# Performance work log

Hardware: AMD Instinct MI355X
Metric: run time of the kernel (lower is better)

Reference implementation:

```python
import jax, jax.numpy as jnp
import numpy as np

N_NODES = 50000
N_EDGES = 800000
N_GRAPHS = 512
IN_DIM = 50
H = 128  # hidden_channels


def _init_linear(key, out_dim, in_dim, bias=True):
    k1, k2 = jax.random.split(key)
    bound = 1.0 / np.sqrt(in_dim)
    W = jax.random.uniform(k1, (out_dim, in_dim), jnp.float32, -bound, bound)
    if bias:
        b = jax.random.uniform(k2, (out_dim,), jnp.float32, -bound, bound)
        return W, b
    return W


def setup_inputs() -> dict:
    key = jax.random.key(0)
    ks = jax.random.split(key, 16)
    x = jax.random.normal(ks[0], (N_NODES, IN_DIM), jnp.float32)
    edge_index = jax.random.randint(ks[1], (2, N_EDGES), 0, N_NODES, jnp.int64)
    batch = jnp.sort(jax.random.randint(ks[2], (N_NODES,), 0, N_GRAPHS, jnp.int64))
    Wl1, bl1 = _init_linear(ks[3], H, IN_DIM)
    Wr1 = _init_linear(ks[4], H, IN_DIM, bias=False)
    Wl2, bl2 = _init_linear(ks[5], 2 * H, H)
    Wr2 = _init_linear(ks[6], 2 * H, H, bias=False)
    Wl3, bl3 = _init_linear(ks[7], 4 * H, 2 * H)
    Wr3 = _init_linear(ks[8], 4 * H, 2 * H, bias=False)
    Wf1, bf1 = _init_linear(ks[9], 2 * H, 4 * H)
    Wf2, bf2 = _init_linear(ks[10], H, 2 * H)
    Wo, bo = _init_linear(ks[11], 1, H)
    return dict(x=x, edge_index=edge_index, batch=batch,
                Wl1=Wl1, bl1=bl1, Wr1=Wr1,
                Wl2=Wl2, bl2=bl2, Wr2=Wr2,
                Wl3=Wl3, bl3=bl3, Wr3=Wr3,
                Wf1=Wf1, bf1=bf1, Wf2=Wf2, bf2=bf2, Wo=Wo, bo=bo)


def sage_conv(x, src, dst, deg_inv, Wl, bl, Wr):
    # mean-aggregate neighbor features at destination nodes, then linear
    agg = jax.ops.segment_sum(x[src], dst, num_segments=N_NODES) * deg_inv
    return agg @ Wl.T + bl + x @ Wr.T


def reference(x, edge_index, batch, Wl1, bl1, Wr1, Wl2, bl2, Wr2,
              Wl3, bl3, Wr3, Wf1, bf1, Wf2, bf2, Wo, bo):
    src, dst = edge_index[0], edge_index[1]
    deg = jax.ops.segment_sum(jnp.ones((N_EDGES,), x.dtype), dst, num_segments=N_NODES)
    deg_inv = (1.0 / jnp.maximum(deg, 1.0))[:, None]

    x1 = jax.nn.leaky_relu(sage_conv(x, src, dst, deg_inv, Wl1, bl1, Wr1))
    x2 = jax.nn.relu(sage_conv(x1, src, dst, deg_inv, Wl2, bl2, Wr2))
    x3 = jax.nn.relu(sage_conv(x2, src, dst, deg_inv, Wl3, bl3, Wr3))

    # global mean pool per graph
    pool_sum = jax.ops.segment_sum(x3, batch, num_segments=N_GRAPHS)
    cnt = jax.ops.segment_sum(jnp.ones((N_NODES,), x.dtype), batch, num_segments=N_GRAPHS)
    x_pool = pool_sum / jnp.maximum(cnt, 1.0)[:, None]

    x4 = jax.nn.relu(x_pool @ Wf1.T + bf1)
    x5 = jax.nn.relu(x4 @ Wf2.T + bf2)
    return jax.nn.sigmoid(x5 @ Wo.T + bo)
```

## Files before the change

### kernel.cpp

```cpp
#include <hip/hip_runtime.h>
#include <math.h>

#define N_NODES 50000
#define N_EDGES 800000
#define N_GRAPHS 512
#define M_PAD 50176
#define SEG_SZ 6250
#define EPT 8
#define SEG_BLOCKS 391
#define FILL_BLOCKS (SEG_BLOCKS * 8)
#define CAP 64

typedef unsigned char u8;
typedef unsigned short u16;
typedef unsigned int u32;
typedef long i64;
using floatx4 = __attribute__((ext_vector_type(4))) float;
using floatx2 = __attribute__((ext_vector_type(2))) float;

__device__ __forceinline__ u8 f2fp8(float v) {
    return (u8)(__builtin_amdgcn_cvt_pk_fp8_f32(v, v, 0, false) & 0xFF);
}
__device__ __forceinline__ u32 pack4fp8(float a, float b, float c, float d) {
    u32 p = __builtin_amdgcn_cvt_pk_fp8_f32(a, b, 0, false);
    return __builtin_amdgcn_cvt_pk_fp8_f32(c, d, p, true);
}
__device__ __forceinline__ void acc16fp8p(floatx2* acc2, uint4 u) {
    const u32 w[4] = {u.x, u.y, u.z, u.w};
    #pragma unroll
    for (int j = 0; j < 4; ++j) {
        acc2[j * 2 + 0] += __builtin_amdgcn_cvt_pk_f32_fp8((int)w[j], false);
        acc2[j * 2 + 1] += __builtin_amdgcn_cvt_pk_f32_fp8((int)w[j], true);
    }
}

__device__ __forceinline__ void load_lds16(const u8* g, u8* l) {
    __builtin_amdgcn_global_load_lds(
        (const __attribute__((address_space(1))) u32*)g,
        (__attribute__((address_space(3))) u32*)l, 16, 0, 0);
}
template<int N> __device__ __forceinline__ void waitcnt_vm() {
    __builtin_amdgcn_s_waitcnt(0x0F70 | N);
}
__device__ __forceinline__ void raw_barrier() {
    asm volatile("s_barrier" ::: "memory");
}

__global__ __launch_bounds__(256) void prep_kernel(
    const int* __restrict__ src, const int* __restrict__ dst,
    int* __restrict__ cursor, u16* __restrict__ csr,
    const int* __restrict__ batch, int* __restrict__ gstart,
    const float* __restrict__ x,
    const float* __restrict__ Wl1, const float* __restrict__ Wr1,
    const float* __restrict__ Wl2, const float* __restrict__ Wr2,
    const float* __restrict__ Wl3, const float* __restrict__ Wr3,
    const float* __restrict__ Wf1, const float* __restrict__ Wf2,
    u8* __restrict__ abuf1,
    u8* __restrict__ wb1, u8* __restrict__ wb2, u8* __restrict__ wb3,
    float* __restrict__ Wf1T, float* __restrict__ Wf2T)
{
    if (blockIdx.x < FILL_BLOCKS) {
        const int seg = blockIdx.x & 7;
        const int lo = seg * SEG_SZ, hi = lo + SEG_SZ;
        int e = (blockIdx.x >> 3) * (256 * EPT) + threadIdx.x;
        #pragma unroll
        for (int j = 0; j < EPT; ++j, e += 256) {
            if (e < N_EDGES) {
                int d = dst[e];
                if (d >= lo && d < hi) {
                    int p = atomicAdd(&cursor[d], 1);
                    csr[d * CAP + p] = (u16)src[e];
                }
            }
        }
        return;
    }
    const int bx = blockIdx.x - FILL_BLOCKS;
    if (bx < 196) {
        int i = bx * 256 + threadIdx.x;
        if (i >= N_NODES) return;
        int b = batch[i];
        int bp = (i == 0) ? -1 : batch[i - 1];
        for (int g = bp + 1; g <= b; ++g) gstart[g] = i;
        if (i == N_NODES - 1)
            for (int g = b + 1; g <= N_GRAPHS; ++g) gstart[g] = N_NODES;
        return;
    }
    int i = (bx - 196) * 256 + threadIdx.x;
    if (i < N_NODES * 16) {
        int n = i >> 4, c = (i & 15) * 4;
        float v[4];
        #pragma unroll
        for (int j = 0; j < 4; ++j) {
            int cc = c + j;
            v[j] = (cc < 50) ? x[n * 50 + cc] : 0.0f;
        }
        *(u32*)(abuf1 + (size_t)n * 128 + 64 + c) = pack4fp8(v[0], v[1], v[2], v[3]);
        return;
    }
    i -= N_NODES * 16;
    if (i < 128 * 64) {
        int o = i / 64, c = i % 64;
        float vl = (c < 50) ? Wl1[o * 50 + c] : 0.0f;
        float vr = (c < 50) ? Wr1[o * 50 + c] : 0.0f;
        wb1[(size_t)o * 128 + c] = f2fp8(vl);
        wb1[(size_t)o * 128 + 64 + c] = f2fp8(vr);
        return;
    }
    i -= 128 * 64;
    if (i < 256 * 128) {
        int o = i / 128, c = i % 128;
        wb2[(size_t)o * 256 + c] = f2fp8(Wl2[o * 128 + c]);
        wb2[(size_t)o * 256 + 128 + c] = f2fp8(Wr2[o * 128 + c]);
        return;
    }
    i -= 256 * 128;
    if (i < 512 * 256) {
        int o = i / 256, c = i % 256;
        wb3[(size_t)o * 512 + c] = f2fp8(Wl3[o * 256 + c]);
        wb3[(size_t)o * 512 + 256 + c] = f2fp8(Wr3[o * 256 + c]);
        return;
    }
    i -= 512 * 256;
    if (i < 256 * 512) {
        int o = i >> 9, k = i & 511;
        Wf1T[(size_t)k * 256 + o] = Wf1[(size_t)o * 512 + k];
        return;
    }
    i -= 256 * 512;
    if (i < 128 * 256) {
        int o = i >> 8, k = i & 255;
        Wf2T[(size_t)k * 128 + o] = Wf2[(size_t)o * 256 + k];
    }
}

template<int DINP>
__global__ __launch_bounds__(256) void csr_agg_kernel(const int* __restrict__ cnt,
                                                      const u16* __restrict__ csr,
                                                      u8* __restrict__ abuf) {
    constexpr int STRIDE = 2 * DINP;
    constexpr int LPR = DINP / 16;
    constexpr int EPW = 64 / LPR;
    const int wave = threadIdx.x >> 6, lane = threadIdx.x & 63;
    const int n = blockIdx.x * 4 + wave;
    if (n >= N_NODES) return;
    const int sub = lane / LPR;
    const int li = lane % LPR;
    const int deg = cnt[n];
    const int s0 = n * CAP, s1 = s0 + deg;

    floatx2 acc2[8] = {};
    const u8* xin = abuf + DINP;

    int e = s0 + sub;
    for (; e + EPW < s1; e += 2 * EPW) {
        int i0 = csr[e], i1 = csr[e + EPW];
        uint4 u0 = *(const uint4*)(xin + (size_t)i0 * STRIDE + li * 16);
        uint4 u1 = *(const uint4*)(xin + (size_t)i1 * STRIDE + li * 16);
        acc16fp8p(acc2, u0);
        acc16fp8p(acc2, u1);
    }
    for (; e < s1; e += EPW) {
        int i0 = csr[e];
        uint4 u0 = *(const uint4*)(xin + (size_t)i0 * STRIDE + li * 16);
        acc16fp8p(acc2, u0);
    }

    #pragma unroll
    for (int off = 32; off >= LPR; off >>= 1) {
        #pragma unroll
        for (int c = 0; c < 8; ++c) {
            floatx2 o;
            o[0] = __shfl_down(acc2[c][0], off);
            o[1] = __shfl_down(acc2[c][1], off);
            acc2[c] += o;
        }
    }

    if (lane < LPR) {
        float sc = 1.0f / fmaxf((float)deg, 1.0f);
        uint4 o;
        o.x = pack4fp8(acc2[0][0] * sc, acc2[0][1] * sc, acc2[1][0] * sc, acc2[1][1] * sc);
        o.y = pack4fp8(acc2[2][0] * sc, acc2[2][1] * sc, acc2[3][0] * sc, acc2[3][1] * sc);
        o.z = pack4fp8(acc2[4][0] * sc, acc2[4][1] * sc, acc2[5][0] * sc, acc2[5][1] * sc);
        o.w = pack4fp8(acc2[6][0] * sc, acc2[6][1] * sc, acc2[7][0] * sc, acc2[7][1] * sc);
        *(uint4*)(abuf + (size_t)n * STRIDE + li * 16) = o;
    }
}

template<int K, int NB, int ACT>
__global__ __launch_bounds__(256) void gemm_fp8_kernel(
    const u8* __restrict__ A, const u8* __restrict__ W,
    const float* __restrict__ bias,
    u8* __restrict__ out8, int gstride, int goff, int N)
{
    constexpr int NKB = K / 32;
    constexpr int MT = M_PAD / 128;
    constexpr int MCHUNK = MT / 8;
    __shared__ __align__(16) u8 As[3][128 * 32];
    __shared__ __align__(16) u8 Bs[3][128 * 32];

    const int bx = blockIdx.x;
    const int xcd = bx & 7;
    const int seq = bx >> 3;
    const int n = seq % NB;
    const int m = xcd * MCHUNK + seq / NB;
    if (m >= MT) return;
    const int bm = m * 128;
    const int bn = n * 128;

    const int tid = threadIdx.x;
    const int wave = tid >> 6, lane = tid & 63;
    const int wm = (wave & 1) * 64, wn = (wave >> 1) * 64;
    const int lm = lane & 15, lq = lane >> 4;

    const int srow = wave * 32 + (lane >> 1);
    const int scol = ((lane & 1) ^ ((lane >> 3) & 1)) * 16;
    const u8* gA = A + (size_t)(bm + srow) * K + scol;
    const u8* gB = W + (size_t)(bn + srow) * K + scol;
    const int lbase = wave * 32 * 32;

    auto stage = [&](int s, int r) {
        const int ko = s * 32;
        load_lds16(gA + ko, &As[r][lbase]);
        load_lds16(gB + ko, &Bs[r][lbase]);
    };

    floatx4 acc[4][4] = {};

    stage(0, 0);
    stage(1, 1);

    const int csw = (((lq >> 1) ^ ((lm >> 2) & 1)) << 4) + (lq & 1) * 8;

    #pragma unroll
    for (int kb = 0; kb < NKB; ++kb) {
        if (kb + 2 < NKB) stage(kb + 2, (kb + 2) % 3);
        const int rem = NKB - 1 - kb;
        if (rem >= 2)      waitcnt_vm<4>();
        else if (rem == 1) waitcnt_vm<2>();
        else               waitcnt_vm<0>();
        raw_barrier();

        const int r = kb % 3;
        i64 af[4], bfr[4];
        #pragma unroll
        for (int mi = 0; mi < 4; ++mi)
            af[mi] = *(const i64*)&As[r][(wm + mi * 16 + lm) * 32 + csw];
        #pragma unroll
        for (int ni = 0; ni < 4; ++ni)
            bfr[ni] = *(const i64*)&Bs[r][(wn + ni * 16 + lm) * 32 + csw];
        #pragma unroll
        for (int mi = 0; mi < 4; ++mi)
            #pragma unroll
            for (int ni = 0; ni < 4; ++ni)
                acc[mi][ni] = __builtin_amdgcn_mfma_f32_16x16x32_fp8_fp8(
                    af[mi], bfr[ni], acc[mi][ni], 0, 0, 0);
        raw_barrier();
    }

    #pragma unroll
    for (int mi = 0; mi < 4; ++mi) {
        int node0 = bm + wm + mi * 16 + lq * 4;
        #pragma unroll
        for (int ni = 0; ni < 4; ++ni) {
            int o = bn + wn + ni * 16 + lm;
            float bi = bias[o];
            #pragma unroll
            for (int r = 0; r < 4; ++r) {
                int node = node0 + r;
                if (node >= N) continue;
                float v = acc[mi][ni][r] + bi;
                if (ACT == 0) v = (v > 0.0f) ? v : 0.01f * v;
                else          v = fmaxf(v, 0.0f);
                out8[(size_t)node * gstride + goff + o] = f2fp8(v);
            }
        }
    }
}

template<int K, int NB, int ACT>
__global__ __launch_bounds__(256) void gemm64_fp8_kernel(
    const u8* __restrict__ A, const u8* __restrict__ W,
    const float* __restrict__ bias,
    u8* __restrict__ out8, int gstride, int goff, int N)
{
    constexpr int NKB = K / 64;
    constexpr int MT = M_PAD / 128;
    constexpr int MCHUNK = MT / 8;
    __shared__ __align__(16) u8 As[3][128 * 64];
    __shared__ __align__(16) u8 Bs[3][128 * 64];

    const int bx = blockIdx.x;
    const int xcd = bx & 7;
    const int seq = bx >> 3;
    const int n = seq % NB;
    const int m = xcd * MCHUNK + seq / NB;
    if (m >= MT) return;
    const int bm = m * 128;
    const int bn = n * 128;

    const int tid = threadIdx.x;
    const int wave = tid >> 6, lane = tid & 63;
    const int wm = (wave & 1) * 64, wn = (wave >> 1) * 64;
    const int lm = lane & 15, lq = lane >> 4;

    const int srow = wave * 16 + (lane >> 2);
    const int scd  = ((lane & 3) ^ ((srow >> 1) & 3)) << 4;
    const u8* gA = A + (size_t)(bm + srow) * K + scd;
    const u8* gB = W + (size_t)(bn + srow) * K + scd;
    const int lbase = wave * 1024;

    auto stage = [&](int s, int r) {
        const int ko = s * 64;
        load_lds16(gA + ko,                    &As[r][lbase]);
        load_lds16(gA + (size_t)64 * K + ko,   &As[r][lbase + 4096]);
        load_lds16(gB + ko,                    &Bs[r][lbase]);
        load_lds16(gB + (size_t)64 * K + ko,   &Bs[r][lbase + 4096]);
    };

    floatx4 acc[4][4] = {};

    stage(0, 0);
    stage(1, 1);

    const int pr = (lm >> 1) & 3;
    const int c0 = (((lq >> 1) ^ pr) << 4)       + ((lq & 1) << 3);
    const int c1 = (((2 + (lq >> 1)) ^ pr) << 4) + ((lq & 1) << 3);

    #pragma unroll
    for (int kb = 0; kb < NKB; ++kb) {
        if (kb + 2 < NKB) stage(kb + 2, (kb + 2) % 3);
        const int rem = NKB - 1 - kb;
        if (rem >= 2)      waitcnt_vm<8>();
        else if (rem == 1) waitcnt_vm<4>();
        else               waitcnt_vm<0>();
        raw_barrier();

        const int r = kb % 3;
        i64 af[4][2], bfr[4][2];
        #pragma unroll
        for (int mi = 0; mi < 4; ++mi) {
            const int base = (wm + mi * 16 + lm) * 64;
            af[mi][0] = *(const i64*)&As[r][base + c0];
            af[mi][1] = *(const i64*)&As[r][base + c1];
        }
        #pragma unroll
        for (int ni = 0; ni < 4; ++ni) {
            const int base = (wn + ni * 16 + lm) * 64;
            bfr[ni][0] = *(const i64*)&Bs[r][base + c0];
            bfr[ni][1] = *(const i64*)&Bs[r][base + c1];
        }
        #pragma unroll
        for (int mi = 0; mi < 4; ++mi)
            #pragma unroll
            for (int ni = 0; ni < 4; ++ni) {
                acc[mi][ni] = __builtin_amdgcn_mfma_f32_16x16x32_fp8_fp8(
                    af[mi][0], bfr[ni][0], acc[mi][ni], 0, 0, 0);
                acc[mi][ni] = __builtin_amdgcn_mfma_f32_16x16x32_fp8_fp8(
                    af[mi][1], bfr[ni][1], acc[mi][ni], 0, 0, 0);
            }
        raw_barrier();
    }

    #pragma unroll
    for (int mi = 0; mi < 4; ++mi) {
        int node0 = bm + wm + mi * 16 + lq * 4;
        #pragma unroll
        for (int ni = 0; ni < 4; ++ni) {
            int o = bn + wn + ni * 16 + lm;
            float bi = bias[o];
            #pragma unroll
            for (int r = 0; r < 4; ++r) {
                int node = node0 + r;
                if (node >= N) continue;
                float v = acc[mi][ni][r] + bi;
                if (ACT == 0) v = (v > 0.0f) ? v : 0.01f * v;
                else          v = fmaxf(v, 0.0f);
                out8[(size_t)node * gstride + goff + o] = f2fp8(v);
            }
        }
    }
}

__global__ __launch_bounds__(256) void pool_kernel(
    const u8* __restrict__ x3, const int* __restrict__ gstart,
    float* __restrict__ pool)
{
    __shared__ float sacc[32][128];
    const int g = blockIdx.x >> 2;
    const int slab = blockIdx.x & 3;
    const int t = threadIdx.x;
    const int chain = t >> 3;
    const int li = t & 7;
    const int c0 = slab * 128 + li * 16;
    const int n0 = gstart[g], n1 = gstart[g + 1];

    floatx2 acc2[8] = {};
    for (int n = n0 + chain; n < n1; n += 32) {
        uint4 u = *(const uint4*)(x3 + (size_t)n * 512 + c0);
        acc16fp8p(acc2, u);
    }
    #pragma unroll
    for (int c = 0; c < 8; ++c) {
        sacc[chain][li * 16 + c * 2 + 0] = acc2[c][0];
        sacc[chain][li * 16 + c * 2 + 1] = acc2[c][1];
    }
    __syncthreads();
    if (t < 128) {
        float s = 0.0f;
        #pragma unroll
        for (int r = 0; r < 32; ++r) s += sacc[r][t];
        pool[(size_t)g * 512 + slab * 128 + t] = s;
    }
}

__global__ __launch_bounds__(256) void dense_head_kernel(
    const float* __restrict__ pool, const int* __restrict__ gstart,
    const float* __restrict__ Wf1T, const float* __restrict__ bf1,
    const float* __restrict__ Wf2T, const float* __restrict__ bf2,
    const float* __restrict__ Wo,  const float* __restrict__ bo,
    float* __restrict__ out)
{
    __shared__ float sp[4][512];
    __shared__ float s4[4][256];
    __shared__ float red[128][4];
    const int g0 = blockIdx.x * 4;
    const int t = threadIdx.x;

    #pragma unroll
    for (int g = 0; g < 4; ++g) {
        float sc = 1.0f / fmaxf((float)(gstart[g0 + g + 1] - gstart[g0 + g]), 1.0f);
        sp[g][t]       = pool[(size_t)(g0 + g) * 512 + t] * sc;
        sp[g][t + 256] = pool[(size_t)(g0 + g) * 512 + 256 + t] * sc;
    }
    __syncthreads();

    {
        float s[4];
        #pragma unroll
        for (int g = 0; g < 4; ++g) s[g] = bf1[t];
        #pragma unroll 8
        for (int k = 0; k < 512; ++k) {
            float w = Wf1T[(size_t)k * 256 + t];
            #pragma unroll
            for (int g = 0; g < 4; ++g) s[g] += sp[g][k] * w;
        }
        #pragma unroll
        for (int g = 0; g < 4; ++g) s4[g][t] = fmaxf(s[g], 0.0f);
    }
    __syncthreads();
    if (t < 128) {
        float s[4];
        #pragma unroll
        for (int g = 0; g < 4; ++g) s[g] = bf2[t];
        #pragma unroll 8
        for (int k = 0; k < 256; ++k) {
            float w = Wf2T[(size_t)k * 128 + t];
            #pragma unroll
            for (int g = 0; g < 4; ++g) s[g] += s4[g][k] * w;
        }
        float wo = Wo[t];
        #pragma unroll
        for (int g = 0; g < 4; ++g) red[t][g] = fmaxf(s[g], 0.0f) * wo;
    }
    __syncthreads();
    for (int off = 64; off >= 1; off >>= 1) {
        if (t < off) {
            #pragma unroll
            for (int g = 0; g < 4; ++g) red[t][g] += red[t + off][g];
        }
        __syncthreads();
    }
    if (t < 4) out[g0 + t] = 1.0f / (1.0f + expf(-(red[0][t] + bo[0])));
}

extern "C" void kernel_launch(void* const* d_in, const int* in_sizes, int n_in,
                              void* d_out, int out_size, void* d_ws, size_t ws_size,
                              hipStream_t stream)
{
    const float* x     = (const float*)d_in[0];
    const int*   ei    = (const int*)  d_in[1];
    const int*   batch = (const int*)  d_in[2];
    const float* Wl1   = (const float*)d_in[3];
    const float* bl1   = (const float*)d_in[4];
    const float* Wr1   = (const float*)d_in[5];
    const float* Wl2   = (const float*)d_in[6];
    const float* bl2   = (const float*)d_in[7];
    const float* Wr2   = (const float*)d_in[8];
    const float* Wl3   = (const float*)d_in[9];
    const float* bl3   = (const float*)d_in[10];
    const float* Wr3   = (const float*)d_in[11];
    const float* Wf1   = (const float*)d_in[12];
    const float* bf1   = (const float*)d_in[13];
    const float* Wf2   = (const float*)d_in[14];
    const float* bf2   = (const float*)d_in[15];
    const float* Wo    = (const float*)d_in[16];
    const float* bo    = (const float*)d_in[17];

    const int* src = ei;
    const int* dst = ei + N_EDGES;

    char* p = (char*)d_ws;
    auto alloc = [&](size_t bytes) { char* r = p; p += (bytes + 255) & ~(size_t)255; return r; };
    int*   gstart = (int*)  alloc(513 * 4);
    float* pool   = (float*)alloc((size_t)512 * 512 * 4);
    float* Wf1T   = (float*)alloc((size_t)512 * 256 * 4);
    float* Wf2T   = (float*)alloc((size_t)256 * 128 * 4);
    u8*    abuf1  = (u8*)   alloc((size_t)M_PAD * 128);
    u8*    abuf2  = (u8*)   alloc((size_t)M_PAD * 256);
    u8*    abuf3  = (u8*)   alloc((size_t)M_PAD * 512);
    u8*    x3buf8 = (u8*)   alloc((size_t)M_PAD * 512);
    u8*    wb1    = (u8*)   alloc((size_t)128 * 128);
    u8*    wb2    = (u8*)   alloc((size_t)256 * 256);
    u8*    wb3    = (u8*)   alloc((size_t)512 * 512);
    int*   cursor = (int*)  alloc(50176 * 4);
    u16*   csr    = (u16*)  alloc((size_t)50176 * CAP * 2);

    hipMemsetAsync(cursor, 0, 50176 * 4, stream);
    const int CONV_N = N_NODES * 16 + 128 * 64 + 256 * 128 + 512 * 256
                     + 256 * 512 + 128 * 256;
    const int CONV_BLOCKS = (CONV_N + 255) / 256;
    prep_kernel<<<FILL_BLOCKS + 196 + CONV_BLOCKS, 256, 0, stream>>>(
        src, dst, cursor, csr,
        batch, gstart, x, Wl1, Wr1, Wl2, Wr2, Wl3, Wr3, Wf1, Wf2,
        abuf1, wb1, wb2, wb3, Wf1T, Wf2T);

    const int GB = 12500;
    const int GEMM_GRID = 49 * 8;

    csr_agg_kernel<64><<<GB, 256, 0, stream>>>(cursor, csr, abuf1);
    gemm_fp8_kernel<128, 1, 0><<<GEMM_GRID * 1, 256, 0, stream>>>(
        abuf1, wb1, bl1, abuf2, 256, 128, N_NODES);

    csr_agg_kernel<128><<<GB, 256, 0, stream>>>(cursor, csr, abuf2);
    gemm64_fp8_kernel<256, 2, 1><<<GEMM_GRID * 2, 256, 0, stream>>>(
        abuf2, wb2, bl2, abuf3, 512, 256, N_NODES);

    csr_agg_kernel<256><<<GB, 256, 0, stream>>>(cursor, csr, abuf3);
    gemm64_fp8_kernel<512, 4, 1><<<GEMM_GRID * 4, 256, 0, stream>>>(
        abuf3, wb3, bl3, x3buf8, 512, 0, N_NODES);

    pool_kernel<<<N_GRAPHS * 4, 256, 0, stream>>>(x3buf8, gstart, pool);
    dense_head_kernel<<<N_GRAPHS / 4, 256, 0, stream>>>(
        pool, gstart, Wf1T, bf1, Wf2T, bf2, Wo, bo, (float*)d_out);
}
```

Baseline: 334.4 us.

## Build CSR per segment with LDS atomics in eight blocks, drop cursor memset

Replaces the many-block CSR fill, which used global atomics on the cursor array, with 8 blocks. Each block owns one destination segment, scans all edges, and counts neighbours with shared-memory atomics. It then writes the final counts to cursor, so the separate memset is no longer needed. The aim is to remove global atomic contention and one extra launch. The cost is that each of the 8 blocks reads the whole edge list with very little parallelism, which can make the prep kernel serial and bandwidth-limited per block.

```diff
diff --git a/kernel.cpp b/kernel.cpp
--- a/kernel.cpp
+++ b/kernel.cpp
@@ -6,9 +6,7 @@
 #define N_GRAPHS 512
 #define M_PAD 50176
 #define SEG_SZ 6250
-#define EPT 8
-#define SEG_BLOCKS 391
-#define FILL_BLOCKS (SEG_BLOCKS * 8)
+#define E_MAIN 798720
 #define CAP 64
 
 typedef unsigned char u8;
@@ -59,23 +57,43 @@
     u8* __restrict__ wb1, u8* __restrict__ wb2, u8* __restrict__ wb3,
     float* __restrict__ Wf1T, float* __restrict__ Wf2T)
 {
-    if (blockIdx.x < FILL_BLOCKS) {
-        const int seg = blockIdx.x & 7;
-        const int lo = seg * SEG_SZ, hi = lo + SEG_SZ;
-        int e = (blockIdx.x >> 3) * (256 * EPT) + threadIdx.x;
-        #pragma unroll
-        for (int j = 0; j < EPT; ++j, e += 256) {
-            if (e < N_EDGES) {
-                int d = dst[e];
-                if (d >= lo && d < hi) {
-                    int p = atomicAdd(&cursor[d], 1);
-                    csr[d * CAP + p] = (u16)src[e];
+    __shared__ int cnt[SEG_SZ];
+
+    if (blockIdx.x < 8) {
+        const int seg = blockIdx.x;
+        const int lo = seg * SEG_SZ;
+        for (int i = threadIdx.x; i < SEG_SZ; i += 256) cnt[i] = 0;
+        __syncthreads();
+
+        for (int base = 0; base < E_MAIN; base += 2048) {
+            const int e = base + threadIdx.x;
+            int dd[8], ss[8];
+            #pragma unroll
+            for (int j = 0; j < 8; ++j) {
+                dd[j] = dst[e + j * 256];
+                ss[j] = src[e + j * 256];
+            }
+            #pragma unroll
+            for (int j = 0; j < 8; ++j) {
+                unsigned d = (unsigned)(dd[j] - lo);
+                if (d < SEG_SZ) {
+                    int p = atomicAdd(&cnt[d], 1);
+                    csr[(size_t)(lo + (int)d) * CAP + p] = (u16)ss[j];
                 }
             }
         }
-        return;
-    }
-    const int bx = blockIdx.x - FILL_BLOCKS;
+        for (int e = E_MAIN + threadIdx.x; e < N_EDGES; e += 256) {
+            unsigned d = (unsigned)(dst[e] - lo);
+            if (d < SEG_SZ) {
+                int p = atomicAdd(&cnt[d], 1);
+                csr[(size_t)(lo + (int)d) * CAP + p] = (u16)src[e];
+            }
+        }
+        __syncthreads();
+        for (int i = threadIdx.x; i < SEG_SZ; i += 256) cursor[lo + i] = cnt[i];
+        return;
+    }
+    const int bx = blockIdx.x - 8;
     if (bx < 196) {
         int i = bx * 256 + threadIdx.x;
         if (i >= N_NODES) return;
@@ -517,11 +535,10 @@
     int*   cursor = (int*)  alloc(50176 * 4);
     u16*   csr    = (u16*)  alloc((size_t)50176 * CAP * 2);
 
-    hipMemsetAsync(cursor, 0, 50176 * 4, stream);
     const int CONV_N = N_NODES * 16 + 128 * 64 + 256 * 128 + 512 * 256
                      + 256 * 512 + 128 * 256;
     const int CONV_BLOCKS = (CONV_N + 255) / 256;
-    prep_kernel<<<FILL_BLOCKS + 196 + CONV_BLOCKS, 256, 0, stream>>>(
+    prep_kernel<<<8 + 196 + CONV_BLOCKS, 256, 0, stream>>>(
         src, dst, cursor, csr,
         batch, gstart, x, Wl1, Wr1, Wl2, Wr2, Wl3, Wr3, Wf1, Wf2,
         abuf1, wb1, wb2, wb3, Wf1T, Wf2T);
```

New measurement: 778.6 us. +132.8%, slower.
